# Kernel tuning notes

Hardware: AMD Instinct MI355X
Metric: run time of the kernel (lower is better)

## Reference

```python
import jax, jax.numpy as jnp
import numpy as np

B, T, N, C = 4, 6, 512, 8
HID, FEAT, EMB, IN_DIM = 64, 16, 32, 1
KS, KC, HORIZON = 3, 2, 3
ALPHA = 3.0

def _init(key, shape):
    fin = shape[-2] if len(shape) >= 2 else shape[-1]
    return jax.random.normal(key, shape, dtype=jnp.float32) * (1.0 / fin) ** 0.5

def setup_inputs():
    ks = jax.random.split(jax.random.key(0), 32)
    L_enc = (IN_DIM + FEAT + HID) * KS * KC
    L_dec = (HID + FEAT + HID) * KS * KC
    return {
        "X_seq": jax.random.normal(ks[0], (B, T, N, C), dtype=jnp.float32),
        "As": jax.random.uniform(ks[1], (N, N), dtype=jnp.float32) / N,
        "Ac": jax.random.uniform(ks[2], (C, C), dtype=jnp.float32) / C,
        "feature": jax.random.normal(ks[3], (N, FEAT), dtype=jnp.float32),
        "Wu_S": _init(ks[4], (C, HID)), "Wv_S": _init(ks[5], (C, HID)),
        "Wu_C": _init(ks[6], (N, HID)), "Wv_C": _init(ks[7], (N, HID)),
        "mfS_w1": _init(ks[8], (4, 2, 256)), "mfS_b1": jnp.zeros((4, 256), jnp.float32),
        "mfS_w2": _init(ks[9], (4, 256, 256)), "mfS_b2": jnp.zeros((4, 256), jnp.float32),
        "mfC_w1": _init(ks[10], (4, 2, 256)), "mfC_b1": jnp.zeros((4, 256), jnp.float32),
        "mfC_w2": _init(ks[11], (4, 256, 256)), "mfC_b2": jnp.zeros((4, 256), jnp.float32),
        "enc_gW": _init(ks[12], (L_enc, 2 * HID)), "enc_gb": jnp.zeros((2 * HID,), jnp.float32),
        "enc_cW": _init(ks[13], (L_enc, HID)), "enc_cb": jnp.zeros((HID,), jnp.float32),
        "dec_gW": _init(ks[14], (L_dec, 2 * HID)), "dec_gb": jnp.zeros((2 * HID,), jnp.float32),
        "dec_cW": _init(ks[15], (L_dec, HID)), "dec_cb": jnp.zeros((HID,), jnp.float32),
        "out_w1": _init(ks[16], (HID, EMB)), "out_b1": jnp.zeros((EMB,), jnp.float32),
        "out_w2": _init(ks[17], (EMB, IN_DIM)), "out_b2": jnp.zeros((IN_DIM,), jnp.float32),
    }

def _mlp(x, w1, b1, w2, b2):
    return jax.nn.relu(x @ w1 + b1) @ w2 + b2

def _mixed_fusion(A, P, w1, b1, w2, b2):
    # node_feat = [rowsum(A), rowsum(P)]; key/value MLPs indexed 0:key_A 1:key_P 2:val_A 3:val_P
    nf = jnp.stack([A.sum(-1), P.sum(-1)], axis=-1)            # [n, 2]
    An, Pn = A @ nf, P @ nf
    key = _mlp(An, w1[0], b1[0], w2[0], b2[0]) + _mlp(Pn, w1[1], b1[1], w2[1], b2[1])
    val = _mlp(An, w1[2], b1[2], w2[2], b2[2]) + _mlp(Pn, w1[3], b1[3], w2[3], b2[3])
    a = jax.nn.sigmoid(key @ val.T)
    return a * A + (1.0 - a) * P

def _adaptive_graph(Xf, Wu, Wv):
    U = jnp.tanh(ALPHA * Xf @ Wu)                              # [b,t,n,h]
    V = jnp.tanh(ALPHA * Xf @ Wv)
    M = jnp.einsum('btnh,btmh->nm', U, V)
    # Ps = softmax(relu(M - M^T)) matches einsum pair in torch source
    return jax.nn.softmax(jax.nn.relu(M - M.T), axis=-1)

def _cheby(G, K):
    mats = [jnp.eye(G.shape[0], dtype=G.dtype), G]
    for _ in range(2, K):
        mats.append(2.0 * G @ mats[-1] - mats[-2])
    return jnp.stack(mats[:K], axis=0)                         # [K, n, n]

def _bdg(X, Gs_set, Gc_set, W, b):
    # X: [b,n,c,l]; fused Ks x Kc Chebyshev mode products; cat order (k, j, l) matches torch cat
    t1 = jnp.einsum('bncl,knm->kbmcl', X, Gs_set)
    t2 = jnp.einsum('kbmcl,jcd->bmdkjl', t1, Gc_set)
    feat = t2.reshape(t2.shape[0], t2.shape[1], t2.shape[2], -1)
    return feat @ W + b

def _cell(Xt, Ht, featx, Gs_set, Gc_set, gW, gb, cW, cb):
    XH = jnp.concatenate([Xt, Ht, featx], axis=-1)
    uv = _bdg(XH, Gs_set, Gc_set, gW, gb)
    update = jax.nn.sigmoid(uv[..., :HID])
    reset = jax.nn.sigmoid(uv[..., HID:])
    cand_in = jnp.concatenate([Xt, reset * Ht, featx], axis=-1)
    cand = jnp.tanh(_bdg(cand_in, Gs_set, Gc_set, cW, cb))
    return (1.0 - update) * Ht + update * cand

def _forward(X_seq, As, Ac, feature, Wu_S, Wv_S, Wu_C, Wv_C,
             mfS_w1, mfS_b1, mfS_w2, mfS_b2, mfC_w1, mfC_b1, mfC_w2, mfC_b2,
             enc_gW, enc_gb, enc_cW, enc_cb, dec_gW, dec_gb, dec_cW, dec_cb,
             out_w1, out_b1, out_w2, out_b2):
    # MGP_Gen: adaptive spatial / categorical graphs fused with priors
    Ps = _adaptive_graph(X_seq, Wu_S, Wv_S)
    Gs = _mixed_fusion(As, Ps, mfS_w1, mfS_b1, mfS_w2, mfS_b2)
    Xc = jnp.swapaxes(X_seq, 2, 3)                             # [b,t,c,n]
    Pc = _adaptive_graph(Xc, Wu_C, Wv_C)
    Gc = _mixed_fusion(Ac, Pc, mfC_w1, mfC_b1, mfC_w2, mfC_b2)
    Gs_set, Gc_set = _cheby(Gs, KS), _cheby(Gc, KC)
    featx = jnp.broadcast_to(feature[None, :, None, :], (B, N, C, FEAT))
    X5 = X_seq[..., None]                                      # [b,t,n,c,1]
    Ht = jnp.zeros((B, N, C, HID), dtype=X_seq.dtype)
    for t in range(T):                                         # encoder GRU over history
        Ht = _cell(X5[:, t], Ht, featx, Gs_set, Gc_set, enc_gW, enc_gb, enc_cW, enc_cb)
    deco_in, Hd = Ht, Ht
    outs = []
    for _ in range(HORIZON):
        Hd = _cell(deco_in, Hd, featx, Gs_set, Gc_set, dec_gW, dec_gb, dec_cW, dec_cb)
        outs.append(_mlp(Hd, out_w1, out_b1, out_w2, out_b2))
        deco_in = Hd
    return jnp.stack(outs, axis=1)                             # [b, horizon, n, c, 1]

def reference(X_seq, As, Ac, feature, Wu_S, Wv_S, Wu_C, Wv_C, mfS_w1, mfS_b1, mfS_w2, mfS_b2, mfC_w1, mfC_b1, mfC_w2, mfC_b2, enc_gW, enc_gb, enc_cW, enc_cb, dec_gW, dec_gb, dec_cW, dec_cb, out_w1, out_b1, out_w2, out_b2):
    return _forward(X_seq, As, Ac, feature, Wu_S, Wv_S, Wu_C, Wv_C, mfS_w1, mfS_b1, mfS_w2, mfS_b2, mfC_w1, mfC_b1, mfC_w2, mfC_b2, enc_gW, enc_gb, enc_cW, enc_cb, dec_gW, dec_gb, dec_cW, dec_cb, out_w1, out_b1, out_w2, out_b2)
```

## Files before the change

### kernel.cpp

```cpp
#include <hip/hip_runtime.h>
#include <math.h>

constexpr int kB = 4, kT = 6, kN = 512, kC = 8;
constexpr int kH = 64, kF = 16, kE = 32;
constexpr int kKS = 3, kKC = 2, kHOR = 3;
constexpr int kBT = kB * kT;
constexpr int kRK = kBT * kH;
constexpr int L_ENC = 1 + kH + kF;
constexpr int L_DEC = kH + kH + kF;
constexpr int PL_ENC = 96;
constexpr int PL_DEC = 160;
constexpr int KP_ENC = 3 * PL_ENC;
constexpr int KP_DGF = 288;
constexpr int KP_DEC = 3 * PL_DEC;
constexpr float kALPHA = 3.0f;

typedef unsigned short ushortT;
typedef short short8 __attribute__((ext_vector_type(8)));
typedef float f32x4 __attribute__((ext_vector_type(4)));

__device__ __forceinline__ float sigm(float x) { return 1.0f / (1.0f + __expf(-x)); }

__device__ __forceinline__ ushortT f2bf(float f) {
    union { float f; unsigned int u; } v; v.f = f;
    unsigned int r = v.u + 0x7fffu + ((v.u >> 16) & 1u);
    return (ushortT)(r >> 16);
}

__device__ __forceinline__ void fma44(const float4& a, const float4& b, float acc[4][4]) {
    acc[0][0] += a.x*b.x; acc[0][1] += a.x*b.y; acc[0][2] += a.x*b.z; acc[0][3] += a.x*b.w;
    acc[1][0] += a.y*b.x; acc[1][1] += a.y*b.y; acc[1][2] += a.y*b.z; acc[1][3] += a.y*b.w;
    acc[2][0] += a.z*b.x; acc[2][1] += a.z*b.y; acc[2][2] += a.z*b.z; acc[2][3] += a.z*b.w;
    acc[3][0] += a.w*b.x; acc[3][1] += a.w*b.y; acc[3][2] += a.w*b.z; acc[3][3] += a.w*b.w;
}

__global__ __launch_bounds__(256) void k_prep_all(
    const float* __restrict__ egW, const float* __restrict__ ecW,
    const float* __restrict__ dgW, const float* __restrict__ dcW,
    const float* __restrict__ w2, const float* __restrict__ w2C,
    ushortT* __restrict__ WTg_e, ushortT* __restrict__ WTc_e,
    ushortT* __restrict__ WTg_d, ushortT* __restrict__ WTc_d,
    float* __restrict__ w2tK, float* __restrict__ w2tV, float* __restrict__ w2tC)
{
    int idx = blockIdx.x * 256 + threadIdx.x;
    if (idx < 73728) {
        int qp = idx % KP_ENC, o = idx / KP_ENC;
        int kk = qp / PL_ENC, l = qp - kk * PL_ENC;
        int lo = (l < 64) ? l + 1 : (l == 64) ? 0 : (l < 80) ? L_ENC : (l - 15);
        int j = o / 128, oo = o - j * 128;
        float v = (lo < L_ENC) ? egW[(size_t)((kk*2 + j)*L_ENC + lo) * 128 + oo] : 0.f;
        WTg_e[idx] = f2bf(v);
    } else if (idx < 110592) {
        int r = idx - 73728;
        int qp = r % KP_ENC, o = r / KP_ENC;
        int kk = qp / PL_ENC, l = qp - kk * PL_ENC;
        int lo = (l < 64) ? l + 1 : (l == 64) ? 0 : (l < 80) ? L_ENC : (l - 15);
        int j = o / 64, oo = o - j * 64;
        float v = (lo < L_ENC) ? ecW[(size_t)((kk*2 + j)*L_ENC + lo) * 64 + oo] : 0.f;
        WTc_e[r] = f2bf(v);
    } else if (idx < 184320) {
        int r = idx - 110592;
        int qp = r % KP_DGF, o = r / KP_DGF;
        int k = qp / 96, p = qp - k * 96;
        int j = o >> 7, oo = o & 127;
        int base = (k*2 + j) * L_DEC;
        float v;
        if (p < 64)      v = dgW[(size_t)(base + p)*128 + oo] + dgW[(size_t)(base + 64 + p)*128 + oo];
        else if (p < 80) v = dgW[(size_t)(base + 128 + (p - 64))*128 + oo];
        else             v = 0.f;
        WTg_d[r] = f2bf(v);
    } else if (idx < 245760) {
        int r = idx - 184320;
        int qp = r % KP_DEC, o = r / KP_DEC;
        int kk = qp / PL_DEC, l = qp - kk * PL_DEC;
        int j = o / 64, oo = o - j * 64;
        float v = (l < L_DEC) ? dcW[(size_t)((kk*2 + j)*L_DEC + l) * 64 + oo] : 0.f;
        WTc_d[r] = f2bf(v);
    } else if (idx < 376832) {
        int r = idx - 245760;
        int kk = r & 511, n = r >> 9;
        int j = kk >> 8, k = kk & 255;
        w2tK[r] = w2[(size_t)(0 + j)*65536 + k*256 + n];
        w2tV[r] = w2[(size_t)(2 + j)*65536 + k*256 + n];
    } else if (idx < 638976) {
        int r = idx - 376832;
        int q = r >> 16; int rem = r & 65535;
        int oc = rem >> 8, k = rem & 255;
        w2tC[r] = w2C[(size_t)q*65536 + k*256 + oc];
    }
}


__global__ __launch_bounds__(256) void k_uvproj_s_nfa(
    const float* __restrict__ X, const float* __restrict__ Wu, const float* __restrict__ Wv,
    const float* __restrict__ As,
    float* __restrict__ Upr, float* __restrict__ Vpr, float* __restrict__ nf)
{
    if (blockIdx.x >= 3072) {
        int i = blockIdx.x - 3072, tid = threadIdx.x;
        __shared__ float sa[256];
        float a = 0.f;
        for (int j = tid; j < kN; j += 256) a += As[(size_t)i*kN + j];
        sa[tid] = a; __syncthreads();
        for (int s = 128; s > 0; s >>= 1) { if (tid < s) sa[tid] += sa[tid+s]; __syncthreads(); }
        if (!tid) { nf[i*2] = sa[0]; nf[i*2+1] = 1.0f; }
        return;
    }
    int idx = blockIdx.x * 256 + threadIdx.x;
    int h = idx % kH; int bt = (idx / kH) % kBT; int n = idx / (kH * kBT);
    const float* xr = X + ((size_t)bt * kN + n) * kC;
    float u = 0.f, v = 0.f;
#pragma unroll
    for (int c = 0; c < kC; ++c) { float x = xr[c]; u += x * Wu[c*kH + h]; v += x * Wv[c*kH + h]; }
    Upr[(size_t)n * kRK + bt * kH + h] = tanhf(kALPHA * u);
    Vpr[(size_t)n * kRK + bt * kH + h] = tanhf(kALPHA * v);
}

__global__ __launch_bounds__(512) void k_uvproj_c2(
    const float* __restrict__ X, const float* __restrict__ WuC, const float* __restrict__ WvC,
    float* __restrict__ Uc, float* __restrict__ Vc)
{
    __shared__ float Xs[4096];
    __shared__ float Wus[4096], Wvs[4096];
    int bt = blockIdx.x, tid = threadIdx.x;
    for (int i = tid; i < 4096; i += 512) Xs[i] = X[(size_t)bt*4096 + i];
    int c = tid >> 6, h = tid & 63;
    float u = 0.f, v = 0.f;
    for (int n0 = 0; n0 < 512; n0 += 64) {
        __syncthreads();
        for (int i = tid; i < 4096; i += 512) { Wus[i] = WuC[n0*64 + i]; Wvs[i] = WvC[n0*64 + i]; }
        __syncthreads();
#pragma unroll 8
        for (int nn = 0; nn < 64; ++nn) {
            float x = Xs[(n0+nn)*8 + c];
            u += x * Wus[nn*64 + h];
            v += x * Wvs[nn*64 + h];
        }
    }
    Uc[(size_t)bt*512 + c*64 + h] = tanhf(kALPHA * u);
    Vc[(size_t)bt*512 + c*64 + h] = tanhf(kALPHA * v);
}

__global__ __launch_bounds__(256) void k_softmax_anpn(
    const float* __restrict__ part, const float* __restrict__ A, const float* __restrict__ nf,
    float* __restrict__ P, float* __restrict__ An, float* __restrict__ Pn)
{
    int i = blockIdx.x, tid = threadIdx.x;
    __shared__ float s0[256], s1[256], s2[256], s3[256], s4[256];
    auto mval = [&](int r, int c2) -> float {
        size_t id = (size_t)r*kN + c2;
        return part[id] + part[262144 + id] + part[524288 + id] + part[786432 + id];
    };
    float mx = -1e30f;
    for (int j = tid; j < kN; j += 256)
        mx = fmaxf(mx, fmaxf(mval(i, j) - mval(j, i), 0.f));
    s0[tid] = mx; __syncthreads();
    for (int s = 128; s > 0; s >>= 1) { if (tid < s) s0[tid] = fmaxf(s0[tid], s0[tid+s]); __syncthreads(); }
    mx = s0[0]; __syncthreads();
    float sum=0, pn0=0, pn1=0, an0=0, an1=0;
    for (int j = tid; j < kN; j += 256) {
        float v = fmaxf(mval(i, j) - mval(j, i), 0.f);
        float e = __expf(v - mx);
        P[(size_t)i*kN + j] = e;
        float n0 = nf[2*j], n1 = nf[2*j+1];
        float a = A[(size_t)i*kN + j];
        sum += e; pn0 += e*n0; pn1 += e*n1; an0 += a*n0; an1 += a*n1;
    }
    s0[tid]=sum; s1[tid]=pn0; s2[tid]=pn1; s3[tid]=an0; s4[tid]=an1; __syncthreads();
    for (int s = 128; s > 0; s >>= 1) {
        if (tid < s) { s0[tid]+=s0[tid+s]; s1[tid]+=s1[tid+s]; s2[tid]+=s2[tid+s]; s3[tid]+=s3[tid+s]; s4[tid]+=s4[tid+s]; }
        __syncthreads();
    }
    float inv = 1.f / s0[0];
    if (!tid) { Pn[i*2] = s1[0]*inv; Pn[i*2+1] = s2[0]*inv; An[i*2] = s3[0]; An[i*2+1] = s4[0]; }
    __syncthreads();
    for (int j = tid; j < kN; j += 256) P[(size_t)i*kN + j] *= inv;
}

__global__ __launch_bounds__(256) void k_mlp1kv(
    const float* __restrict__ An, const float* __restrict__ Pn,
    const float* __restrict__ w1, const float* __restrict__ b1, float* __restrict__ hid)
{
    int idx = blockIdx.x * 256 + threadIdx.x;
    if (idx >= 524288) return;
    int half = idx >> 18;
    int r = idx & 262143;
    int col = r & 511, i = r >> 9;
    int ia = half*2, ip = half*2 + 1;
    float v;
    if (col < 256) {
        const float* w = w1 + (size_t)ia * 512;
        v = An[i*2]*w[col] + An[i*2+1]*w[256 + col] + b1[ia*256 + col];
    } else {
        int o = col - 256;
        const float* w = w1 + (size_t)ip * 512;
        v = Pn[i*2]*w[o] + Pn[i*2+1]*w[256 + o] + b1[ip*256 + o];
    }
    hid[idx] = fmaxf(v, 0.f);
}

__global__ __launch_bounds__(256) void k_gemm_ntsk(
    const float* __restrict__ A, const float* __restrict__ B, float* __restrict__ part,
    int M, int N, int K, int skl)
{
    __shared__ __align__(16) float sA[32][68];
    __shared__ __align__(16) float sB[32][68];
    int tid = threadIdx.x, tx = tid & 15, ty = tid >> 4;
    int j0 = blockIdx.x * 64, i0 = blockIdx.y * 64;
    int kb = blockIdx.z * skl;
    float acc[4][4] = {};
    for (int k0 = kb; k0 < kb + skl; k0 += 32) {
#pragma unroll
        for (int it = 0; it < 2; ++it) {
            int q = tid + it * 256;
            int row = q >> 3, ks = (q & 7) * 4;
            float4 va = *(const float4*)&A[(size_t)(i0 + row)*K + k0 + ks];
            float4 vb = *(const float4*)&B[(size_t)(j0 + row)*K + k0 + ks];
            sA[ks+0][row] = va.x; sA[ks+1][row] = va.y; sA[ks+2][row] = va.z; sA[ks+3][row] = va.w;
            sB[ks+0][row] = vb.x; sB[ks+1][row] = vb.y; sB[ks+2][row] = vb.z; sB[ks+3][row] = vb.w;
        }
        __syncthreads();
#pragma unroll
        for (int kk = 0; kk < 32; ++kk) {
            float4 a = *(const float4*)&sA[kk][ty*4];
            float4 b = *(const float4*)&sB[kk][tx*4];
            fma44(a, b, acc);
        }
        __syncthreads();
    }
    float* dst = part + (size_t)blockIdx.z * M * N;
#pragma unroll
    for (int i = 0; i < 4; ++i)
#pragma unroll
        for (int j = 0; j < 4; ++j)
            dst[(size_t)(i0 + ty*4 + i)*N + j0 + tx*4 + j] = acc[i][j];
}

__global__ __launch_bounds__(256) void k_ntsk_kv(
    const float* __restrict__ hid, const float* __restrict__ w2t, float* __restrict__ part)
{
    __shared__ __align__(16) float sA[32][68];
    __shared__ __align__(16) float sB[32][68];
    int tid = threadIdx.x, tx = tid & 15, ty = tid >> 4;
    int z = blockIdx.z;
    const float* A = hid + (size_t)(z >> 1) * 262144;
    const float* B = w2t + (size_t)(z >> 1) * 131072;
    int kb = (z & 1) * 256;
    int j0 = blockIdx.x * 64, i0 = blockIdx.y * 64;
    float acc[4][4] = {};
    for (int k0 = kb; k0 < kb + 256; k0 += 32) {
#pragma unroll
        for (int it = 0; it < 2; ++it) {
            int q = tid + it * 256;
            int row = q >> 3, ks = (q & 7) * 4;
            float4 va = *(const float4*)&A[(size_t)(i0 + row)*512 + k0 + ks];
            float4 vb = *(const float4*)&B[(size_t)(j0 + row)*512 + k0 + ks];
            sA[ks+0][row] = va.x; sA[ks+1][row] = va.y; sA[ks+2][row] = va.z; sA[ks+3][row] = va.w;
            sB[ks+0][row] = vb.x; sB[ks+1][row] = vb.y; sB[ks+2][row] = vb.z; sB[ks+3][row] = vb.w;
        }
        __syncthreads();
#pragma unroll
        for (int kk = 0; kk < 32; ++kk) {
            float4 a = *(const float4*)&sA[kk][ty*4];
            float4 b = *(const float4*)&sB[kk][tx*4];
            fma44(a, b, acc);
        }
        __syncthreads();
    }
    float* dst = part + (size_t)z * 131072;
#pragma unroll
    for (int i = 0; i < 4; ++i)
#pragma unroll
        for (int j = 0; j < 4; ++j)
            dst[(size_t)(i0 + ty*4 + i)*256 + j0 + tx*4 + j] = acc[i][j];
}

__global__ __launch_bounds__(256) void k_redep_kv(
    const float* __restrict__ part, const float* __restrict__ b2, float* __restrict__ keyval)
{
    int idx = blockIdx.x * 256 + threadIdx.x;
    if (idx >= 262144) return;
    int half = idx >> 17, off = idx & 131071, col = idx & 255;
    float s = part[(size_t)(half*2)*131072 + off] + part[(size_t)(half*2 + 1)*131072 + off];
    s += b2[half*512 + col] + b2[half*512 + 256 + col];
    keyval[idx] = s;
}

__global__ void k_fuse_transp(
    const float* __restrict__ part, const float* __restrict__ As,
    const float* __restrict__ Ps, ushortT* __restrict__ Gt)
{
    __shared__ float tile[32][33];
    int bx = blockIdx.x * 32, by = blockIdx.y * 32;
    int x = threadIdx.x, y0 = threadIdx.y;
    for (int yy = y0; yy < 32; yy += 8) {
        size_t id = (size_t)(by + yy)*kN + bx + x;
        float s = part[id] + part[262144 + id];
        float a = sigm(s);
        tile[yy][x] = a*As[id] + (1.f - a)*Ps[id];
    }
    __syncthreads();
    for (int yy = y0; yy < 32; yy += 8) Gt[(size_t)(bx+yy)*kN + by + x] = f2bf(tile[x][yy]);
}

__global__ __launch_bounds__(256) void k_cheby64(
    const ushortT* __restrict__ Gst, ushortT* __restrict__ Gst2)
{
    __shared__ short sA[64][40];
    __shared__ short sB[64][40];
    int tid = threadIdx.x;
    int m0 = blockIdx.y * 64, j0 = blockIdx.x * 64;
    int w = tid >> 6, lane = tid & 63;
    f32x4 acc[4];
#pragma unroll
    for (int i = 0; i < 4; ++i) acc[i] = (f32x4){0.f, 0.f, 0.f, 0.f};
    for (int k0 = 0; k0 < kN; k0 += 32) {
        {
            int row = tid >> 2, lc = (tid & 3) * 8;
            *(short8*)&sA[row][lc] = *(const short8*)(Gst + (size_t)(m0 + row)*kN + k0 + lc);
        }
        {
            int kr = tid & 31, jc = (tid >> 5) * 8;
            short8 v = *(const short8*)(Gst + (size_t)(k0 + kr)*kN + j0 + jc);
#pragma unroll
            for (int i = 0; i < 8; ++i) sB[jc + i][kr] = v[i];
        }
        __syncthreads();
        short8 bf = *(const short8*)&sB[w*16 + (lane & 15)][(lane >> 4) * 8];
#pragma unroll
        for (int mi = 0; mi < 4; ++mi) {
            short8 af = *(const short8*)&sA[mi*16 + (lane & 15)][(lane >> 4) * 8];
            acc[mi] = __builtin_amdgcn_mfma_f32_16x16x32_bf16(af, bf, acc[mi], 0, 0, 0);
        }
        __syncthreads();
    }
#pragma unroll
    for (int mi = 0; mi < 4; ++mi) {
        int row0 = m0 + mi*16 + (lane >> 4)*4;
        int col = j0 + w*16 + (lane & 15);
#pragma unroll
        for (int q = 0; q < 4; ++q) {
            int row = row0 + q;
            Gst2[(size_t)row*kN + col] = f2bf(2.f*acc[mi][q] - (row == col ? 1.f : 0.f));
        }
    }
}

__device__ __forceinline__ void cat_front2(
    const float* __restrict__ Uc, const float* __restrict__ Vc, const float* __restrict__ Ac,
    float* UVs , float* red ,
    float* McS, float* Pcs, float* rsA, float* Ans, float* Pns)
{
    int tid = threadIdx.x;
    int cd = tid >> 2, kc = tid & 3;
    int c = cd >> 3, d = cd & 7;
    float s = 0.f;
    for (int bt0 = 0; bt0 < kBT; bt0 += 4) {
        __syncthreads();
        for (int i = tid; i < 2048; i += 256) {
            UVs[i]        = Uc[(size_t)bt0*512 + i];
            UVs[2048 + i] = Vc[(size_t)bt0*512 + i];
        }
        __syncthreads();
#pragma unroll
        for (int bt = 0; bt < 4; ++bt)
#pragma unroll
            for (int hh = 0; hh < 16; ++hh) {
                int h = kc*16 + hh;
                s += UVs[bt*512 + c*64 + h] * UVs[2048 + bt*512 + d*64 + h];
            }
    }
    red[tid] = s; __syncthreads();
    if (tid < 64) McS[tid] = red[tid*4] + red[tid*4+1] + red[tid*4+2] + red[tid*4+3];
    __syncthreads();
    if (tid < 8) {
        int i = tid;
        float row[8]; float mx = -1e30f;
#pragma unroll
        for (int j = 0; j < 8; ++j) { float v = fmaxf(McS[i*8+j] - McS[j*8+i], 0.f); row[j] = v; mx = fmaxf(mx, v); }
        float s2 = 0.f;
#pragma unroll
        for (int j = 0; j < 8; ++j) { row[j] = __expf(row[j] - mx); s2 += row[j]; }
        float inv = 1.f / s2;
#pragma unroll
        for (int j = 0; j < 8; ++j) Pcs[i*8+j] = row[j] * inv;
        float a = 0.f;
#pragma unroll
        for (int j = 0; j < 8; ++j) a += Ac[i*8+j];
        rsA[i] = a;
    }
    __syncthreads();
    if (tid < 16) {
        int i = tid >> 1, comp = tid & 1;
        float an = 0.f, pn = 0.f;
#pragma unroll
        for (int j = 0; j < 8; ++j) {
            float nfj = comp ? 1.f : rsA[j];
            an += Ac[i*8+j] * nfj; pn += Pcs[i*8+j] * nfj;
        }
        Ans[i*2+comp] = an; Pns[i*2+comp] = pn;
    }
    __syncthreads();
}

__global__ __launch_bounds__(256) void k_catmlp4(
    const float* __restrict__ Uc, const float* __restrict__ Vc, const float* __restrict__ Ac,
    const float* __restrict__ w1, const float* __restrict__ b1,
    const float* __restrict__ w2tC, const float* __restrict__ b2,
    float* __restrict__ keyval)
{
    __shared__ float UVs[4096];
    __shared__ float red[256];
    __shared__ float McS[64], Pcs[64], rsA[8], Ans[16], Pns[16];
    __shared__ float hA[8][260], hP[8][260];
    int tid = threadIdx.x;
    int kv = blockIdx.x, c0 = blockIdx.y * 32;
    int qa = kv*2, qp = kv*2 + 1;
    cat_front2(Uc, Vc, Ac, UVs, red, McS, Pcs, rsA, Ans, Pns);
    for (int e = tid; e < 2048; e += 256) {
        int i = e >> 8, o = e & 255;
        hA[i][o] = fmaxf(Ans[i*2]*w1[qa*512 + o] + Ans[i*2+1]*w1[qa*512 + 256 + o] + b1[qa*256 + o], 0.f);
        hP[i][o] = fmaxf(Pns[i*2]*w1[qp*512 + o] + Pns[i*2+1]*w1[qp*512 + 256 + o] + b1[qp*256 + o], 0.f);
    }
    __syncthreads();
    int i = tid >> 5, ocl = tid & 31, oc = c0 + ocl;
    float s = b2[qa*256 + oc] + b2[qp*256 + oc];
    const float* wa = w2tC + (size_t)qa*65536 + (size_t)oc*256;
    const float* wp = w2tC + (size_t)qp*65536 + (size_t)oc*256;
#pragma unroll 4
    for (int k = 0; k < 256; k += 4) {
        float4 va = *(const float4*)&wa[k];
        float4 vp = *(const float4*)&wp[k];
        float4 ha = *(const float4*)&hA[i][k];
        float4 hp = *(const float4*)&hP[i][k];
        s += va.x*ha.x + va.y*ha.y + va.z*ha.z + va.w*ha.w
           + vp.x*hp.x + vp.y*hp.y + vp.z*hp.z + vp.w*hp.w;
    }
    keyval[(size_t)kv*2048 + i*256 + oc] = s;
}

__global__ __launch_bounds__(256) void k_gcfuse4(
    const float* __restrict__ keyval,
    const float* __restrict__ Uc, const float* __restrict__ Vc, const float* __restrict__ Ac,
    float* __restrict__ GcF)
{
    __shared__ float UVs[4096];
    __shared__ float red[256];
    __shared__ float McS[64], Pcs[64], rsA[8], Ans[16], Pns[16];
    __shared__ float dotp[256];
    int tid = threadIdx.x;
    cat_front2(Uc, Vc, Ac, UVs, red, McS, Pcs, rsA, Ans, Pns);
    int cd = tid >> 2, kc = tid & 3;
    int c = cd >> 3, d = cd & 7;
    const float* key = keyval;
    const float* val = keyval + 2048;
    float s = 0.f;
#pragma unroll 4
    for (int k = kc*64; k < kc*64 + 64; k += 4) {
        float4 k4 = *(const float4*)&key[c*256 + k];
        float4 v4 = *(const float4*)&val[d*256 + k];
        s += k4.x*v4.x + k4.y*v4.y + k4.z*v4.z + k4.w*v4.w;
    }
    dotp[tid] = s; __syncthreads();
    if (tid < 64) {
        float t = dotp[tid*4] + dotp[tid*4+1] + dotp[tid*4+2] + dotp[tid*4+3];
        float a = sigm(t);
        GcF[tid] = a*Ac[tid] + (1.f - a)*Pcs[tid];
    }
}

template<int CLP, int PL, int ACTW, int OFF>
__global__ __launch_bounds__(256) void k_t1m(
    const ushortT* __restrict__ Gst, const ushortT* __restrict__ Xin, ushortT* __restrict__ Yout)
{
    __shared__ short sA[128][40];
    __shared__ short sB[128][40];
    int tid = threadIdx.x;
    int ki = blockIdx.z >> 2, b = blockIdx.z & 3;
    const ushortT* A = Gst + (size_t)ki * kN * kN;
    const ushortT* B = Xin + (size_t)b * kN * CLP;
    ushortT* C = Yout + (size_t)(ki*4 + b) * kN * CLP;
    int m0 = blockIdx.y * 128, j0 = blockIdx.x * 128;
    int w = tid >> 6, lane = tid & 63, wr = w >> 1, wc = w & 1;
    int kr = tid & 31, jc = (tid >> 5) * 8;
    int colr0, colr1;
    { int j = j0 + jc;      int cg = j / ACTW; colr0 = cg*PL + OFF + (j - cg*ACTW); }
    { int j = j0 + jc + 64; int cg = j / ACTW; colr1 = cg*PL + OFF + (j - cg*ACTW); }
    f32x4 acc[4][4];
#pragma unroll
    for (int i = 0; i < 4; ++i)
#pragma unroll
        for (int j = 0; j < 4; ++j) acc[i][j] = (f32x4){0.f, 0.f, 0.f, 0.f};

    for (int k0 = 0; k0 < kN; k0 += 32) {
        {
            int row = tid >> 1, lc = (tid & 1) * 16;
            const ushortT* p = A + (size_t)(m0 + row)*kN + k0 + lc;
            *(short8*)&sA[row][lc]     = *(const short8*)p;
            *(short8*)&sA[row][lc + 8] = *(const short8*)(p + 8);
        }
        {
            short8 v0 = *(const short8*)(B + (size_t)(k0 + kr)*CLP + colr0);
            short8 v1 = *(const short8*)(B + (size_t)(k0 + kr)*CLP + colr1);
#pragma unroll
            for (int i = 0; i < 8; ++i) sB[jc + i][kr] = v0[i];
#pragma unroll
            for (int i = 0; i < 8; ++i) sB[jc + 64 + i][kr] = v1[i];
        }
        __syncthreads();
        short8 af[4], bfr[4];
#pragma unroll
        for (int mi = 0; mi < 4; ++mi)
            af[mi] = *(const short8*)&sA[wr*64 + mi*16 + (lane & 15)][(lane >> 4) * 8];
#pragma unroll
        for (int ni = 0; ni < 4; ++ni)
            bfr[ni] = *(const short8*)&sB[wc*64 + ni*16 + (lane & 15)][(lane >> 4) * 8];
#pragma unroll
        for (int mi = 0; mi < 4; ++mi)
#pragma unroll
            for (int ni = 0; ni < 4; ++ni)
                acc[mi][ni] = __builtin_amdgcn_mfma_f32_16x16x32_bf16(af[mi], bfr[ni], acc[mi][ni], 0, 0, 0);
        __syncthreads();
    }
#pragma unroll
    for (int mi = 0; mi < 4; ++mi) {
#pragma unroll
        for (int ni = 0; ni < 4; ++ni) {
            int row = m0 + wr*64 + mi*16 + (lane >> 4) * 4;
            int fj = j0 + wc*64 + ni*16;
            int cg = fj / ACTW;
            int col = cg*PL + OFF + (fj - cg*ACTW) + (lane & 15);
#pragma unroll
            for (int q = 0; q < 4; ++q)
                C[(size_t)(row + q)*CLP + col] = f2bf(acc[mi][ni][q]);
        }
    }
}

template<int PL, int NQ, int MODE, int FN>
__global__ __launch_bounds__(256) void k_gg(
    const ushortT* __restrict__ XH, const ushortT* __restrict__ Yb,
    const ushortT* __restrict__ WT, float* __restrict__ Cout)
{
    constexpr int BN = 32 * FN;
    constexpr int KP = NQ * 32;
    constexpr int Ntot = 64 * FN;
    __shared__ short sA[128][40];
    __shared__ short sB[BN][40];
    int tid = threadIdx.x;
    int r0 = blockIdx.y * 128, j0 = blockIdx.x * BN;
    int b = r0 >> 12, rr = r0 & 4095;
    const ushortT* src0 = XH + (size_t)r0 * PL;
    const ushortT* src1 = Yb + ((size_t)b       * 4096 + rr) * PL;
    const ushortT* src2 = Yb + ((size_t)(4 + b) * 4096 + rr) * PL;
    int w = tid >> 6, lane = tid & 63, wr = w >> 1, wc = w & 1;
    f32x4 acc[4][FN];
#pragma unroll
    for (int i = 0; i < 4; ++i)
#pragma unroll
        for (int j = 0; j < FN; ++j) acc[i][j] = (f32x4){0.f, 0.f, 0.f, 0.f};

    for (int q = 0; q < NQ; ++q) {
        int k, off;
        if (MODE == 0)      { k = q/3; off = (q - k*3)*32; }
        else if (MODE == 1) { k = q/3; int part = q - k*3; off = (part < 2) ? part*32 : 128; }
        else                { k = q/5; off = (q - k*5)*32; }
        const ushortT* Ap = (k == 0) ? src0 : (k == 1) ? src1 : src2;
        {
            int row = tid >> 1, lc = (tid & 1) * 16;
            const ushortT* p = Ap + (size_t)row * PL + off + lc;
            *(short8*)&sA[row][lc]     = *(const short8*)p;
            *(short8*)&sA[row][lc + 8] = *(const short8*)(p + 8);
        }
        if (FN == 4) {
            int col = tid >> 1, seg = (tid & 1) * 16;
            const ushortT* p = WT + (size_t)(j0 + col)*KP + q*32 + seg;
            *(short8*)&sB[col][seg]     = *(const short8*)p;
            *(short8*)&sB[col][seg + 8] = *(const short8*)(p + 8);
        } else {
            int col = tid >> 2, seg = (tid & 3) * 8;
            *(short8*)&sB[col][seg] = *(const short8*)(WT + (size_t)(j0 + col)*KP + q*32 + seg);
        }
        __syncthreads();
        short8 af[4], bfr[FN];
#pragma unroll
        for (int mi = 0; mi < 4; ++mi)
            af[mi] = *(const short8*)&sA[wr*64 + mi*16 + (lane & 15)][(lane >> 4) * 8];
#pragma unroll
        for (int ni = 0; ni < FN; ++ni)
            bfr[ni] = *(const short8*)&sB[wc*16*FN + ni*16 + (lane & 15)][(lane >> 4) * 8];
#pragma unroll
        for (int mi = 0; mi < 4; ++mi)
#pragma unroll
            for (int ni = 0; ni < FN; ++ni)
                acc[mi][ni] = __builtin_amdgcn_mfma_f32_16x16x32_bf16(af[mi], bfr[ni], acc[mi][ni], 0, 0, 0);
        __syncthreads();
    }
#pragma unroll
    for (int mi = 0; mi < 4; ++mi) {
#pragma unroll
        for (int ni = 0; ni < FN; ++ni) {
            int row = r0 + wr*64 + mi*16 + (lane >> 4) * 4;
            int col = j0 + wc*16*FN + ni*16 + (lane & 15);
#pragma unroll
            for (int q = 0; q < 4; ++q)
                Cout[(size_t)(row + q)*Ntot + col] = acc[mi][ni][q];
        }
    }
}


template<int PL, int XOFF>
__global__ __launch_bounds__(256) void k_gates_ep(
    const float* __restrict__ Gg, const float* __restrict__ GcM,
    const float* __restrict__ gb, const float* __restrict__ Ht,
    float* __restrict__ upd, ushortT* __restrict__ XH)
{
    __shared__ float sG[8][256];
    __shared__ float GcS[64];
    int tid = threadIdx.x, bm = blockIdx.x;
    const float* src = Gg + (size_t)bm * 2048;
    for (int i = tid; i < 2048; i += 256) sG[i >> 8][i & 255] = src[i];
    if (tid < 64) GcS[tid] = GcM[tid];
    __syncthreads();
    int d = tid >> 5, o0 = (tid & 31) * 4;
    size_t rb = (size_t)bm * 8 + d;
#pragma unroll
    for (int q = 0; q < 4; ++q) {
        int o = o0 + q;
        float pre = sG[d][o] + gb[o];
#pragma unroll
        for (int c = 0; c < 8; ++c) pre += GcS[c*8 + d] * sG[c][128 + o];
        float g = sigm(pre);
        if (o < kH) upd[rb*kH + o] = g;
        else {
            int h = o - kH;
            XH[rb*PL + XOFF + h] = f2bf(g * Ht[rb*kH + h]);
        }
    }
}

template<int MODE>
__global__ __launch_bounds__(256) void k_cand_ep(
    const float* __restrict__ Gc2, const float* __restrict__ GcM,
    const float* __restrict__ cb, const float* __restrict__ upd,
    float* __restrict__ Ht, ushortT* __restrict__ XHo,
    const float* __restrict__ X, int tnext,
    const float* __restrict__ ow1, const float* __restrict__ ob1,
    const float* __restrict__ ow2, const float* __restrict__ ob2,
    float* __restrict__ out, int hz)
{
    __shared__ float sG[8][128];
    __shared__ float GcS[64];
    __shared__ float Hn[8][65];
    __shared__ float Pp[8][32];
    int tid = threadIdx.x, bm = blockIdx.x;
    const float* src = Gc2 + (size_t)bm * 1024;
    for (int i = tid; i < 1024; i += 256) sG[i >> 7][i & 127] = src[i];
    if (tid < 64) GcS[tid] = GcM[tid];
    __syncthreads();
    int d = tid >> 5, o0 = (tid & 31) * 2;
    size_t rb = (size_t)bm * 8 + d;
#pragma unroll
    for (int jj = 0; jj < 2; ++jj) {
        int o = o0 + jj;
        float pre = sG[d][o] + cb[o];
#pragma unroll
        for (int c = 0; c < 8; ++c) pre += GcS[c*8 + d] * sG[c][64 + o];
        float cv = tanhf(pre);
        float u = upd[rb*kH + o];
        float h0 = Ht[rb*kH + o];
        float hn = (1.f - u)*h0 + u*cv;
        Ht[rb*kH + o] = hn;
        if (MODE >= 2) Hn[d][o] = hn;
        if (MODE == 0)      XHo[rb*PL_ENC + o] = f2bf(hn);
        else if (MODE <= 2) XHo[rb*PL_DEC + o] = f2bf(hn);
    }
    if (MODE == 0) {
        if (tid < 8) {
            int r = bm*8 + tid;
            int c2 = r & 7, m = (r >> 3) & 511, b2 = r >> 12;
            XHo[(size_t)r*PL_ENC + 64] = f2bf(X[(((size_t)b2*kT + tnext)*kN + m)*kC + c2]);
        }
    }
    if (MODE >= 2) {
        __syncthreads();
        int row = tid >> 5, e = tid & 31;
        float s = ob1[e];
#pragma unroll
        for (int k = 0; k < kH; ++k) s += Hn[row][k] * ow1[k*kE + e];
        Pp[row][e] = fmaxf(s, 0.f) * ow2[e];
        __syncthreads();
        if (tid < 8) {
            float v = ob2[0];
#pragma unroll
            for (int e2 = 0; e2 < 32; ++e2) v += Pp[tid][e2];
            int r = bm*8 + tid;
            int c2 = r & 7, m = (r >> 3) & 511, b2 = r >> 12;
            out[((size_t)(b2*kHOR + hz)*kN + m)*kC + c2] = v;
        }
    }
}

__global__ __launch_bounds__(256) void k_build_init(
    const float* __restrict__ X, const float* __restrict__ featr,
    ushortT* __restrict__ XHe, ushortT* __restrict__ XHd, float* __restrict__ Ht)
{
    int idx = blockIdx.x * 256 + threadIdx.x;
    if (idx < 1572864) {
        int l = idx % PL_ENC; int r = idx / PL_ENC;
        float v;
        if (l < 64)       v = 0.f;
        else if (l == 64) { int c = r & 7, m = (r >> 3) & 511, b = r >> 12; v = X[(((size_t)b*kT)*kN + m)*kC + c]; }
        else if (l < 80)  v = 0.f;
        else              { int m = (r >> 3) & 511; v = featr[m*kF + (l - 80)]; }
        XHe[idx] = f2bf(v);
    } else if (idx < 2097152) {
        int r2 = idx - 1572864;
        int l2 = r2 & 31; int r = r2 >> 5;
        float v = (l2 < 16) ? featr[((r >> 3) & 511)*kF + l2] : 0.f;
        XHd[(size_t)r*PL_DEC + 128 + l2] = f2bf(v);
    } else if (idx < 3145728) {
        Ht[idx - 2097152] = 0.f;
    }
}

extern "C" void kernel_launch(void* const* d_in, const int* in_sizes, int n_in,
                              void* d_out, int out_size, void* d_ws, size_t ws_size,
                              hipStream_t stream)
{
    (void)in_sizes; (void)n_in; (void)out_size; (void)ws_size;
    const float* X      = (const float*)d_in[0];
    const float* As     = (const float*)d_in[1];
    const float* Ac     = (const float*)d_in[2];
    const float* featr  = (const float*)d_in[3];
    const float* WuS    = (const float*)d_in[4];
    const float* WvS    = (const float*)d_in[5];
    const float* WuC    = (const float*)d_in[6];
    const float* WvC    = (const float*)d_in[7];
    const float* mfS_w1 = (const float*)d_in[8];
    const float* mfS_b1 = (const float*)d_in[9];
    const float* mfS_w2 = (const float*)d_in[10];
    const float* mfS_b2 = (const float*)d_in[11];
    const float* mfC_w1 = (const float*)d_in[12];
    const float* mfC_b1 = (const float*)d_in[13];
    const float* mfC_w2 = (const float*)d_in[14];
    const float* mfC_b2 = (const float*)d_in[15];
    const float* enc_gW = (const float*)d_in[16];
    const float* enc_gb = (const float*)d_in[17];
    const float* enc_cW = (const float*)d_in[18];
    const float* enc_cb = (const float*)d_in[19];
    const float* dec_gW = (const float*)d_in[20];
    const float* dec_gb = (const float*)d_in[21];
    const float* dec_cW = (const float*)d_in[22];
    const float* dec_cb = (const float*)d_in[23];
    const float* out_w1 = (const float*)d_in[24];
    const float* out_b1 = (const float*)d_in[25];
    const float* out_w2 = (const float*)d_in[26];
    const float* out_b2 = (const float*)d_in[27];
    float* out = (float*)d_out;
    float* ws = (float*)d_ws;

    float* Ht     = ws;
    float* updb   = Ht + 1048576;
    float* Gg     = updb + 1048576;
    float* Gs_pad = Gg + 4194304;
    float* smallf = Gs_pad + 262144;
    float* nfS = smallf;
    float* AnS = nfS + 1024;
    float* PnS = AnS + 1024;
    float* GcF = PnS + 1024;
    float* kvC = GcF + 64;
    ushortT* XHb  = (ushortT*)(smallf + 8192);
    ushortT* Yb   = XHb + 2621440;
    ushortT* GstB = Yb + 5242880;
    ushortT* WTg_e = GstB + 524288;
    ushortT* WTc_e = WTg_e + 73728;
    ushortT* WTg_d = WTc_e + 36864;
    ushortT* WTc_d = WTg_d + 122880;
    ushortT* XHd   = WTc_d + 61440;
    float* Upr   = Gg;
    float* Vpr   = Upr + 786432;
    float* part  = Vpr + 786432;
    float* Ps    = part + 1048576;
    float* hidKV = Ps + 262144;
    float* keyval= hidKV + 524288;
    float* w2tKV = keyval + 262144;
    float* w2tC  = w2tKV + 262144;
    float* Uc    = updb;
    float* Vc    = Uc + 12288;

    constexpr int CLP_ENC = kC * PL_ENC;
    constexpr int CLP_DEC = kC * PL_DEC;

    k_prep_all<<<2496, 256, 0, stream>>>(enc_gW, enc_cW, dec_gW, dec_cW, mfS_w2, mfC_w2,
                                         WTg_e, WTc_e, WTg_d, WTc_d,
                                         w2tKV, w2tKV + 131072, w2tC);

    k_uvproj_s_nfa<<<3584, 256, 0, stream>>>(X, WuS, WvS, As, Upr, Vpr, nfS);
    k_gemm_ntsk<<<dim3(8, 8, 4), 256, 0, stream>>>(Upr, Vpr, part, 512, 512, 1536, 384);
    k_softmax_anpn<<<kN, 256, 0, stream>>>(part, As, nfS, Ps, AnS, PnS);
    k_mlp1kv<<<2048, 256, 0, stream>>>(AnS, PnS, mfS_w1, mfS_b1, hidKV);
    k_ntsk_kv<<<dim3(4, 8, 4), 256, 0, stream>>>(hidKV, w2tKV, part);
    k_redep_kv<<<1024, 256, 0, stream>>>(part, mfS_b2, keyval);
    k_gemm_ntsk<<<dim3(8, 8, 2), 256, 0, stream>>>(keyval, keyval + 131072, part, 512, 512, 256, 128);
    k_fuse_transp<<<dim3(16, 16), dim3(32, 8), 0, stream>>>(part, As, Ps, GstB);
    k_cheby64<<<dim3(8, 8), 256, 0, stream>>>(GstB, GstB + 262144);

    k_uvproj_c2<<<kBT, 512, 0, stream>>>(X, WuC, WvC, Uc, Vc);
    k_catmlp4<<<dim3(2, 8), 256, 0, stream>>>(Uc, Vc, Ac, mfC_w1, mfC_b1, w2tC, mfC_b2, kvC);
    k_gcfuse4<<<1, 256, 0, stream>>>(kvC, Uc, Vc, Ac, GcF);

    k_build_init<<<12288, 256, 0, stream>>>(X, featr, XHb, XHd, Ht);

    for (int t = 0; t < kT; ++t) {
        if (t == 0)
            k_t1m<CLP_ENC, PL_ENC, 96, 0><<<dim3(6, 4, 8), 256, 0, stream>>>(GstB, XHb, Yb);
        else
            k_t1m<CLP_ENC, PL_ENC, 80, 0><<<dim3(5, 4, 8), 256, 0, stream>>>(GstB, XHb, Yb);
        k_gg<PL_ENC, 9, 0, 4><<<dim3(2, 128), 256, 0, stream>>>(XHb, Yb, WTg_e, Gg);
        k_gates_ep<PL_ENC, 0><<<2048, 256, 0, stream>>>(Gg, GcF, enc_gb, Ht, updb, XHb);
        k_t1m<CLP_ENC, PL_ENC, 64, 0><<<dim3(4, 4, 8), 256, 0, stream>>>(GstB, XHb, Yb);
        k_gg<PL_ENC, 9, 0, 2><<<dim3(2, 128), 256, 0, stream>>>(XHb, Yb, WTc_e, Gg);
        if (t < kT - 1)
            k_cand_ep<0><<<2048, 256, 0, stream>>>(Gg, GcF, enc_cb, updb, Ht, XHb, X, t + 1,
                                                   nullptr, nullptr, nullptr, nullptr, nullptr, 0);
        else
            k_cand_ep<1><<<2048, 256, 0, stream>>>(Gg, GcF, enc_cb, updb, Ht, XHd, nullptr, 0,
                                                   nullptr, nullptr, nullptr, nullptr, nullptr, 0);
    }

    k_t1m<CLP_DEC, PL_DEC, 16, 128><<<dim3(1, 4, 8), 256, 0, stream>>>(GstB, XHd, Yb);
    for (int hz = 0; hz < kHOR; ++hz) {
        k_t1m<CLP_DEC, PL_DEC, 64, 0><<<dim3(4, 4, 8), 256, 0, stream>>>(GstB, XHd, Yb);
        k_gg<PL_DEC, 9, 1, 4><<<dim3(2, 128), 256, 0, stream>>>(XHd, Yb, WTg_d, Gg);
        k_gates_ep<PL_DEC, 64><<<2048, 256, 0, stream>>>(Gg, GcF, dec_gb, Ht, updb, XHd);
        k_t1m<CLP_DEC, PL_DEC, 64, 64><<<dim3(4, 4, 8), 256, 0, stream>>>(GstB, XHd, Yb);
        k_gg<PL_DEC, 15, 2, 2><<<dim3(2, 128), 256, 0, stream>>>(XHd, Yb, WTc_d, Gg);
        if (hz < kHOR - 1)
            k_cand_ep<2><<<2048, 256, 0, stream>>>(Gg, GcF, dec_cb, updb, Ht, XHd, nullptr, 0,
                                                   out_w1, out_b1, out_w2, out_b2, out, hz);
        else
            k_cand_ep<3><<<2048, 256, 0, stream>>>(Gg, GcF, dec_cb, updb, Ht, XHd, nullptr, 0,
                                                   out_w1, out_b1, out_w2, out_b2, out, hz);
    }
}
```

Baseline: 918.3 us.

## Fuse gate and candidate GEMMs with their GRU epilogues into single kernels

Merges the gate GEMM (k_gg) with the sigmoid/reset epilogue, and the candidate GEMM with the tanh/state-update/output-MLP epilogue. Each block now computes the full output width for 128 rows and stages accumulators through a shared-memory union, which removes the fp32 Gg round trip to global memory and two kernel launches per step. The cost is fewer blocks (128 instead of 256 GEMM blocks), more registers per thread (acc[4][8] in the gates kernel) and serialized epilogue chunks, which may lower occupancy on a large-CU device.

```diff
diff --git a/kernel.cpp b/kernel.cpp
--- a/kernel.cpp
+++ b/kernel.cpp
@@ -537,112 +537,110 @@
     }
 }
 
-template<int PL, int NQ, int MODE, int FN>
-__global__ __launch_bounds__(256) void k_gg(
-    const ushortT* __restrict__ XH, const ushortT* __restrict__ Yb,
-    const ushortT* __restrict__ WT, float* __restrict__ Cout)
-{
-    constexpr int BN = 32 * FN;
+union GatesSmem {
+    struct { short A[128][40]; short B[256][40]; } g;
+    float Ep[32][260];
+};
+
+template<int PL, int NQ, int GMODE, int XOFF>
+__global__ __launch_bounds__(256) void k_ggates(
+    ushortT* __restrict__ XH, const ushortT* __restrict__ Yb,
+    const ushortT* __restrict__ WT, const float* __restrict__ GcM,
+    const float* __restrict__ gb, const float* __restrict__ Ht,
+    float* __restrict__ upd)
+{
     constexpr int KP = NQ * 32;
-    constexpr int Ntot = 64 * FN;
-    __shared__ short sA[128][40];
-    __shared__ short sB[BN][40];
+    __shared__ GatesSmem sm;
+    __shared__ float GcS[64], gbS[128];
     int tid = threadIdx.x;
-    int r0 = blockIdx.y * 128, j0 = blockIdx.x * BN;
+    int r0 = blockIdx.x * 128;
     int b = r0 >> 12, rr = r0 & 4095;
     const ushortT* src0 = XH + (size_t)r0 * PL;
     const ushortT* src1 = Yb + ((size_t)b       * 4096 + rr) * PL;
     const ushortT* src2 = Yb + ((size_t)(4 + b) * 4096 + rr) * PL;
+    if (tid < 64) GcS[tid] = GcM[tid];
+    if (tid >= 64 && tid < 192) gbS[tid - 64] = gb[tid - 64];
     int w = tid >> 6, lane = tid & 63, wr = w >> 1, wc = w & 1;
-    f32x4 acc[4][FN];
+    f32x4 acc[4][8];
 #pragma unroll
     for (int i = 0; i < 4; ++i)
 #pragma unroll
-        for (int j = 0; j < FN; ++j) acc[i][j] = (f32x4){0.f, 0.f, 0.f, 0.f};
+        for (int j = 0; j < 8; ++j) acc[i][j] = (f32x4){0.f, 0.f, 0.f, 0.f};
 
     for (int q = 0; q < NQ; ++q) {
         int k, off;
-        if (MODE == 0)      { k = q/3; off = (q - k*3)*32; }
-        else if (MODE == 1) { k = q/3; int part = q - k*3; off = (part < 2) ? part*32 : 128; }
-        else                { k = q/5; off = (q - k*5)*32; }
+        if (GMODE == 0) { k = q/3; off = (q - k*3)*32; }
+        else            { k = q/3; int part = q - k*3; off = (part < 2) ? part*32 : 128; }
         const ushortT* Ap = (k == 0) ? src0 : (k == 1) ? src1 : src2;
         {
             int row = tid >> 1, lc = (tid & 1) * 16;
             const ushortT* p = Ap + (size_t)row * PL + off + lc;
-            *(short8*)&sA[row][lc]     = *(const short8*)p;
-            *(short8*)&sA[row][lc + 8] = *(const short8*)(p + 8);
-        }
-        if (FN == 4) {
-            int col = tid >> 1, seg = (tid & 1) * 16;
-            const ushortT* p = WT + (size_t)(j0 + col)*KP + q*32 + seg;
-            *(short8*)&sB[col][seg]     = *(const short8*)p;
-            *(short8*)&sB[col][seg + 8] = *(const short8*)(p + 8);
-        } else {
-            int col = tid >> 2, seg = (tid & 3) * 8;
-            *(short8*)&sB[col][seg] = *(const short8*)(WT + (size_t)(j0 + col)*KP + q*32 + seg);
-        }
-        __syncthreads();
-        short8 af[4], bfr[FN];
+            *(short8*)&sm.g.A[row][lc]     = *(const short8*)p;
+            *(short8*)&sm.g.A[row][lc + 8] = *(const short8*)(p + 8);
+        }
+        {
+            const ushortT* p = WT + (size_t)tid*KP + q*32;
+            *(short8*)&sm.g.B[tid][0]  = *(const short8*)(p);
+            *(short8*)&sm.g.B[tid][8]  = *(const short8*)(p + 8);
+            *(short8*)&sm.g.B[tid][16] = *(const short8*)(p + 16);
+            *(short8*)&sm.g.B[tid][24] = *(const short8*)(p + 24);
+        }
+        __syncthreads();
+        short8 af[4], bfr[8];
 #pragma unroll
         for (int mi = 0; mi < 4; ++mi)
-            af[mi] = *(const short8*)&sA[wr*64 + mi*16 + (lane & 15)][(lane >> 4) * 8];
-#pragma unroll
-        for (int ni = 0; ni < FN; ++ni)
-            bfr[ni] = *(const short8*)&sB[wc*16*FN + ni*16 + (lane & 15)][(lane >> 4) * 8];
+            af[mi] = *(const short8*)&sm.g.A[wr*64 + mi*16 + (lane & 15)][(lane >> 4) * 8];
+#pragma unroll
+        for (int ni = 0; ni < 8; ++ni)
+            bfr[ni] = *(const short8*)&sm.g.B[wc*128 + ni*16 + (lane & 15)][(lane >> 4) * 8];
 #pragma unroll
         for (int mi = 0; mi < 4; ++mi)
 #pragma unroll
-            for (int ni = 0; ni < FN; ++ni)
+            for (int ni = 0; ni < 8; ++ni)
                 acc[mi][ni] = __builtin_amdgcn_mfma_f32_16x16x32_bf16(af[mi], bfr[ni], acc[mi][ni], 0, 0, 0);
         __syncthreads();
     }
-#pragma unroll
-    for (int mi = 0; mi < 4; ++mi) {
-#pragma unroll
-        for (int ni = 0; ni < FN; ++ni) {
-            int row = r0 + wr*64 + mi*16 + (lane >> 4) * 4;
-            int col = j0 + wc*16*FN + ni*16 + (lane & 15);
-#pragma unroll
-            for (int q = 0; q < 4; ++q)
-                Cout[(size_t)(row + q)*Ntot + col] = acc[mi][ni][q];
-        }
-    }
-}
-
-
-template<int PL, int XOFF>
-__global__ __launch_bounds__(256) void k_gates_ep(
-    const float* __restrict__ Gg, const float* __restrict__ GcM,
-    const float* __restrict__ gb, const float* __restrict__ Ht,
-    float* __restrict__ upd, ushortT* __restrict__ XH)
-{
-    __shared__ float sG[8][256];
-    __shared__ float GcS[64];
-    int tid = threadIdx.x, bm = blockIdx.x;
-    const float* src = Gg + (size_t)bm * 2048;
-    for (int i = tid; i < 2048; i += 256) sG[i >> 8][i & 255] = src[i];
-    if (tid < 64) GcS[tid] = GcM[tid];
-    __syncthreads();
-    int d = tid >> 5, o0 = (tid & 31) * 4;
-    size_t rb = (size_t)bm * 8 + d;
-#pragma unroll
-    for (int q = 0; q < 4; ++q) {
-        int o = o0 + q;
-        float pre = sG[d][o] + gb[o];
-#pragma unroll
-        for (int c = 0; c < 8; ++c) pre += GcS[c*8 + d] * sG[c][128 + o];
-        float g = sigm(pre);
-        if (o < kH) upd[rb*kH + o] = g;
-        else {
-            int h = o - kH;
-            XH[rb*PL + XOFF + h] = f2bf(g * Ht[rb*kH + h]);
-        }
-    }
-}
-
-template<int MODE>
-__global__ __launch_bounds__(256) void k_cand_ep(
-    const float* __restrict__ Gc2, const float* __restrict__ GcM,
+    for (int ch = 0; ch < 4; ++ch) {
+        if (wr == (ch >> 1)) {
+#pragma unroll
+            for (int mi2 = 0; mi2 < 2; ++mi2) {
+                int mi = (ch & 1)*2 + mi2;
+#pragma unroll
+                for (int ni = 0; ni < 8; ++ni)
+#pragma unroll
+                    for (int q = 0; q < 4; ++q)
+                        sm.Ep[mi2*16 + (lane >> 4)*4 + q][wc*128 + ni*16 + (lane & 15)] = acc[mi][ni][q];
+            }
+        }
+        __syncthreads();
+        for (int it = 0; it < 16; ++it) {
+            int idx = it*256 + tid;
+            int o = idx & 127, rloc = idx >> 7;
+            int r = r0 + ch*32 + rloc;
+            int d = r & 7, bb = rloc & ~7;
+            float pre = sm.Ep[rloc][o] + gbS[o];
+#pragma unroll
+            for (int c = 0; c < 8; ++c) pre += GcS[c*8 + d] * sm.Ep[bb + c][128 + o];
+            float g = sigm(pre);
+            if (o < 64) upd[(size_t)r*64 + o] = g;
+            else {
+                int h = o - 64;
+                XH[(size_t)r*PL + XOFF + h] = f2bf(g * Ht[(size_t)r*64 + h]);
+            }
+        }
+        __syncthreads();
+    }
+}
+
+union CandSmem {
+    struct { short A[128][40]; short B[128][40]; } g;
+    struct { float Ep[32][132]; float Hn[32][66]; float Pp[32][33]; } e;
+};
+
+template<int PL, int NQ, int GMODE, int EMODE>
+__global__ __launch_bounds__(256) void k_gcand(
+    const ushortT* __restrict__ XH, const ushortT* __restrict__ Yb,
+    const ushortT* __restrict__ WT, const float* __restrict__ GcM,
     const float* __restrict__ cb, const float* __restrict__ upd,
     float* __restrict__ Ht, ushortT* __restrict__ XHo,
     const float* __restrict__ X, int tnext,
@@ -650,55 +648,114 @@
     const float* __restrict__ ow2, const float* __restrict__ ob2,
     float* __restrict__ out, int hz)
 {
-    __shared__ float sG[8][128];
-    __shared__ float GcS[64];
-    __shared__ float Hn[8][65];
-    __shared__ float Pp[8][32];
-    int tid = threadIdx.x, bm = blockIdx.x;
-    const float* src = Gc2 + (size_t)bm * 1024;
-    for (int i = tid; i < 1024; i += 256) sG[i >> 7][i & 127] = src[i];
+    constexpr int KP = NQ * 32;
+    __shared__ CandSmem sm;
+    __shared__ float GcS[64], cbS[64];
+    int tid = threadIdx.x;
+    int r0 = blockIdx.x * 128;
+    int b = r0 >> 12, rr = r0 & 4095;
+    const ushortT* src0 = XH + (size_t)r0 * PL;
+    const ushortT* src1 = Yb + ((size_t)b       * 4096 + rr) * PL;
+    const ushortT* src2 = Yb + ((size_t)(4 + b) * 4096 + rr) * PL;
     if (tid < 64) GcS[tid] = GcM[tid];
-    __syncthreads();
-    int d = tid >> 5, o0 = (tid & 31) * 2;
-    size_t rb = (size_t)bm * 8 + d;
-#pragma unroll
-    for (int jj = 0; jj < 2; ++jj) {
-        int o = o0 + jj;
-        float pre = sG[d][o] + cb[o];
-#pragma unroll
-        for (int c = 0; c < 8; ++c) pre += GcS[c*8 + d] * sG[c][64 + o];
-        float cv = tanhf(pre);
-        float u = upd[rb*kH + o];
-        float h0 = Ht[rb*kH + o];
-        float hn = (1.f - u)*h0 + u*cv;
-        Ht[rb*kH + o] = hn;
-        if (MODE >= 2) Hn[d][o] = hn;
-        if (MODE == 0)      XHo[rb*PL_ENC + o] = f2bf(hn);
-        else if (MODE <= 2) XHo[rb*PL_DEC + o] = f2bf(hn);
-    }
-    if (MODE == 0) {
-        if (tid < 8) {
-            int r = bm*8 + tid;
-            int c2 = r & 7, m = (r >> 3) & 511, b2 = r >> 12;
-            XHo[(size_t)r*PL_ENC + 64] = f2bf(X[(((size_t)b2*kT + tnext)*kN + m)*kC + c2]);
-        }
-    }
-    if (MODE >= 2) {
-        __syncthreads();
-        int row = tid >> 5, e = tid & 31;
-        float s = ob1[e];
-#pragma unroll
-        for (int k = 0; k < kH; ++k) s += Hn[row][k] * ow1[k*kE + e];
-        Pp[row][e] = fmaxf(s, 0.f) * ow2[e];
-        __syncthreads();
-        if (tid < 8) {
-            float v = ob2[0];
-#pragma unroll
-            for (int e2 = 0; e2 < 32; ++e2) v += Pp[tid][e2];
-            int r = bm*8 + tid;
-            int c2 = r & 7, m = (r >> 3) & 511, b2 = r >> 12;
-            out[((size_t)(b2*kHOR + hz)*kN + m)*kC + c2] = v;
-        }
+    if (tid >= 64 && tid < 128) cbS[tid - 64] = cb[tid - 64];
+    int w = tid >> 6, lane = tid & 63, wr = w >> 1, wc = w & 1;
+    f32x4 acc[4][4];
+#pragma unroll
+    for (int i = 0; i < 4; ++i)
+#pragma unroll
+        for (int j = 0; j < 4; ++j) acc[i][j] = (f32x4){0.f, 0.f, 0.f, 0.f};
+
+    for (int q = 0; q < NQ; ++q) {
+        int k, off;
+        if (GMODE == 0) { k = q/3; off = (q - k*3)*32; }
+        else            { k = q/5; off = (q - k*5)*32; }
+        const ushortT* Ap = (k == 0) ? src0 : (k == 1) ? src1 : src2;
+        {
+            int row = tid >> 1, lc = (tid & 1) * 16;
+            const ushortT* p = Ap + (size_t)row * PL + off + lc;
+            *(short8*)&sm.g.A[row][lc]     = *(const short8*)p;
+            *(short8*)&sm.g.A[row][lc + 8] = *(const short8*)(p + 8);
+        }
+        {
+            int col = tid >> 1, seg = (tid & 1) * 16;
+            const ushortT* p = WT + (size_t)col*KP + q*32 + seg;
+            *(short8*)&sm.g.B[col][seg]     = *(const short8*)p;
+            *(short8*)&sm.g.B[col][seg + 8] = *(const short8*)(p + 8);
+        }
+        __syncthreads();
+        short8 af[4], bfr[4];
+#pragma unroll
+        for (int mi = 0; mi < 4; ++mi)
+            af[mi] = *(const short8*)&sm.g.A[wr*64 + mi*16 + (lane & 15)][(lane >> 4) * 8];
+#pragma unroll
+        for (int ni = 0; ni < 4; ++ni)
+            bfr[ni] = *(const short8*)&sm.g.B[wc*64 + ni*16 + (lane & 15)][(lane >> 4) * 8];
+#pragma unroll
+        for (int mi = 0; mi < 4; ++mi)
+#pragma unroll
+            for (int ni = 0; ni < 4; ++ni)
+                acc[mi][ni] = __builtin_amdgcn_mfma_f32_16x16x32_bf16(af[mi], bfr[ni], acc[mi][ni], 0, 0, 0);
+        __syncthreads();
+    }
+    for (int ch = 0; ch < 4; ++ch) {
+        if (wr == (ch >> 1)) {
+#pragma unroll
+            for (int mi2 = 0; mi2 < 2; ++mi2) {
+                int mi = (ch & 1)*2 + mi2;
+#pragma unroll
+                for (int ni = 0; ni < 4; ++ni)
+#pragma unroll
+                    for (int q = 0; q < 4; ++q)
+                        sm.e.Ep[mi2*16 + (lane >> 4)*4 + q][wc*64 + ni*16 + (lane & 15)] = acc[mi][ni][q];
+            }
+        }
+        __syncthreads();
+        for (int it = 0; it < 8; ++it) {
+            int idx = it*256 + tid;
+            int o = idx & 63, rloc = idx >> 6;
+            int r = r0 + ch*32 + rloc;
+            int d = r & 7, bb = rloc & ~7;
+            float pre = sm.e.Ep[rloc][o] + cbS[o];
+#pragma unroll
+            for (int c = 0; c < 8; ++c) pre += GcS[c*8 + d] * sm.e.Ep[bb + c][64 + o];
+            float cv = tanhf(pre);
+            float u = upd[(size_t)r*64 + o];
+            float h0 = Ht[(size_t)r*64 + o];
+            float hn = (1.f - u)*h0 + u*cv;
+            Ht[(size_t)r*64 + o] = hn;
+            if (EMODE >= 2) sm.e.Hn[rloc][o] = hn;
+            if (EMODE == 0) {
+                XHo[(size_t)r*PL_ENC + o] = f2bf(hn);
+                if (o == 0) {
+                    int c2 = r & 7, m = (r >> 3) & 511, b2 = r >> 12;
+                    XHo[(size_t)r*PL_ENC + 64] = f2bf(X[(((size_t)b2*kT + tnext)*kN + m)*kC + c2]);
+                }
+            } else if (EMODE <= 2) {
+                XHo[(size_t)r*PL_DEC + o] = f2bf(hn);
+            }
+        }
+        if (EMODE >= 2) {
+            __syncthreads();
+            for (int it = 0; it < 4; ++it) {
+                int item = it*256 + tid;
+                int row = item >> 5, e = item & 31;
+                float s = ob1[e];
+#pragma unroll
+                for (int k = 0; k < kH; ++k) s += sm.e.Hn[row][k] * ow1[k*kE + e];
+                sm.e.Pp[row][e] = fmaxf(s, 0.f) * ow2[e];
+            }
+            __syncthreads();
+            if (tid < 32) {
+                float v = ob2[0];
+#pragma unroll
+                for (int e2 = 0; e2 < 32; ++e2) v += sm.e.Pp[tid][e2];
+                int r = r0 + ch*32 + tid;
+                int c2 = r & 7, m = (r >> 3) & 511, b2 = r >> 12;
+                out[((size_t)(b2*kHOR + hz)*kN + m)*kC + c2] = v;
+            }
+        }
+        __syncthreads();
     }
 }
 
@@ -818,30 +875,26 @@
             k_t1m<CLP_ENC, PL_ENC, 96, 0><<<dim3(6, 4, 8), 256, 0, stream>>>(GstB, XHb, Yb);
         else
             k_t1m<CLP_ENC, PL_ENC, 80, 0><<<dim3(5, 4, 8), 256, 0, stream>>>(GstB, XHb, Yb);
-        k_gg<PL_ENC, 9, 0, 4><<<dim3(2, 128), 256, 0, stream>>>(XHb, Yb, WTg_e, Gg);
-        k_gates_ep<PL_ENC, 0><<<2048, 256, 0, stream>>>(Gg, GcF, enc_gb, Ht, updb, XHb);
+        k_ggates<PL_ENC, 9, 0, 0><<<128, 256, 0, stream>>>(XHb, Yb, WTg_e, GcF, enc_gb, Ht, updb);
         k_t1m<CLP_ENC, PL_ENC, 64, 0><<<dim3(4, 4, 8), 256, 0, stream>>>(GstB, XHb, Yb);
-        k_gg<PL_ENC, 9, 0, 2><<<dim3(2, 128), 256, 0, stream>>>(XHb, Yb, WTc_e, Gg);
         if (t < kT - 1)
-            k_cand_ep<0><<<2048, 256, 0, stream>>>(Gg, GcF, enc_cb, updb, Ht, XHb, X, t + 1,
-                                                   nullptr, nullptr, nullptr, nullptr, nullptr, 0);
+            k_gcand<PL_ENC, 9, 0, 0><<<128, 256, 0, stream>>>(XHb, Yb, WTc_e, GcF, enc_cb, updb, Ht,
+                XHb, X, t + 1, nullptr, nullptr, nullptr, nullptr, nullptr, 0);
         else
-            k_cand_ep<1><<<2048, 256, 0, stream>>>(Gg, GcF, enc_cb, updb, Ht, XHd, nullptr, 0,
-                                                   nullptr, nullptr, nullptr, nullptr, nullptr, 0);
+            k_gcand<PL_ENC, 9, 0, 1><<<128, 256, 0, stream>>>(XHb, Yb, WTc_e, GcF, enc_cb, updb, Ht,
+                XHd, nullptr, 0, nullptr, nullptr, nullptr, nullptr, nullptr, 0);
     }
 
     k_t1m<CLP_DEC, PL_DEC, 16, 128><<<dim3(1, 4, 8), 256, 0, stream>>>(GstB, XHd, Yb);
     for (int hz = 0; hz < kHOR; ++hz) {
         k_t1m<CLP_DEC, PL_DEC, 64, 0><<<dim3(4, 4, 8), 256, 0, stream>>>(GstB, XHd, Yb);
-        k_gg<PL_DEC, 9, 1, 4><<<dim3(2, 128), 256, 0, stream>>>(XHd, Yb, WTg_d, Gg);
-        k_gates_ep<PL_DEC, 64><<<2048, 256, 0, stream>>>(Gg, GcF, dec_gb, Ht, updb, XHd);
+        k_ggates<PL_DEC, 9, 1, 64><<<128, 256, 0, stream>>>(XHd, Yb, WTg_d, GcF, dec_gb, Ht, updb);
         k_t1m<CLP_DEC, PL_DEC, 64, 64><<<dim3(4, 4, 8), 256, 0, stream>>>(GstB, XHd, Yb);
-        k_gg<PL_DEC, 15, 2, 2><<<dim3(2, 128), 256, 0, stream>>>(XHd, Yb, WTc_d, Gg);
         if (hz < kHOR - 1)
-            k_cand_ep<2><<<2048, 256, 0, stream>>>(Gg, GcF, dec_cb, updb, Ht, XHd, nullptr, 0,
-                                                   out_w1, out_b1, out_w2, out_b2, out, hz);
+            k_gcand<PL_DEC, 15, 2, 2><<<128, 256, 0, stream>>>(XHd, Yb, WTc_d, GcF, dec_cb, updb, Ht,
+                XHd, nullptr, 0, out_w1, out_b1, out_w2, out_b2, out, hz);
         else
-            k_cand_ep<3><<<2048, 256, 0, stream>>>(Gg, GcF, dec_cb, updb, Ht, XHd, nullptr, 0,
-                                                   out_w1, out_b1, out_w2, out_b2, out, hz);
-    }
-}
+            k_gcand<PL_DEC, 15, 2, 3><<<128, 256, 0, stream>>>(XHd, Yb, WTc_d, GcF, dec_cb, updb, Ht,
+                XHd, nullptr, 0, out_w1, out_b1, out_w2, out_b2, out, hz);
+    }
+}
```

After: 1.494 ms. +62.7%, slower.
